# Kernel optimization log

Hardware: AMD Instinct MI355X
Metric: run time of the kernel (lower is better)

## Reference

```python
import jax, jax.numpy as jnp
import numpy as np

# Fixed quadtree structure for these inputs: base_size=192 => min=12, max=48.
# Level 1 (h=96 > max=48) always partitions; level 2 (h=48) never does because
# binarized uniform uncertainty has density ~0.99 > threshold 0.2.
# => 16 leaf windows of S=48 (N=2304 tokens each), identical to a 4x4 tiling.
B, D, H, W, S = 1, 64, 192, 192, 48
NEG = -1e10


def _to_windows(t, s):
    # [B,C,H,W] -> [B*(H//s)*(W//s), s*s, C]
    b, c, h, w = t.shape
    return t.reshape(b, c, h // s, s, w // s, s).transpose(0, 2, 4, 3, 5, 1).reshape(b * (h // s) * (w // s), s * s, c)


def _from_windows(t, b, c, h, w, s):
    # inverse of _to_windows
    return t.reshape(b, h // s, w // s, s, s, c).transpose(0, 5, 1, 3, 2, 4).reshape(b, c, h, w)


def setup_inputs() -> dict:
    key = jax.random.key(0)
    ks = jax.random.split(key, 16)
    d = D
    sc = 0.1  # ~1/sqrt(d) init scale
    n = lambda k, shape: jax.random.normal(k, shape, jnp.float32) * sc
    return {
        "x": jax.random.normal(ks[0], (B, d, H, W), jnp.float32),
        "reference_features": jax.random.normal(ks[1], (B, d, H, W), jnp.float32),
        "uncertainty_map": jax.random.uniform(ks[2], (B, 1, H, W), jnp.float32),
        "in_proj_w": n(ks[3], (3 * d, d)),
        "in_proj_b": n(ks[4], (3 * d,)),
        "out_proj_w": n(ks[5], (d, d)),
        "out_proj_b": n(ks[6], (d,)),
        "w1": n(ks[7], (d, d)),
        "b1": n(ks[8], (d,)),
        "w3": n(ks[9], (d, d, 3, 3)),
        "b3": n(ks[10], (d,)),
        "w4": n(ks[11], (1, d, 1, 1)),
        "b4": n(ks[12], (1,)),
    }


def reference(x, reference_features, uncertainty_map, in_proj_w, in_proj_b,
              out_proj_w, out_proj_b, w1, b1, w3, b3, w4, b4):
    b, c, h, w = x.shape
    u_bin = jnp.where(uncertainty_map > 0.01, 1.0, 0.0)
    qi = _to_windows(x, S)                      # [BW, N, C]
    kv = _to_windows(reference_features, S)     # [BW, N, C]
    u = _to_windows(u_bin, S)[..., 0]           # [BW, N]

    # torch nn.MultiheadAttention (1 head, batch_first) with additive float mask
    wq, wk, wv = jnp.split(in_proj_w, 3, axis=0)
    bq, bk, bv = jnp.split(in_proj_b, 3, axis=0)
    q = qi @ wq.T + bq
    k = kv @ wk.T + bk
    v = kv @ wv.T + bv
    logits = jnp.einsum('bnd,bmd->bnm', q, k) / (float(c) ** 0.5)
    # attn_mask = -1e10 where outer(u,u) < 1 (i.e. either token not uncertain)
    logits = logits + jnp.where(u[:, :, None] * u[:, None, :] < 1.0, NEG, 0.0)
    attn = jax.nn.softmax(logits, axis=-1)
    o = jnp.einsum('bnm,bmd->bnd', attn, v)
    o = o @ out_proj_w.T + out_proj_b           # MHA out_proj
    o = o @ w1.T + b1                           # conv_out1 (Linear)

    refined = _from_windows(qi + o, b, c, h, w, S)  # residual add per window

    # conv_out3: 3x3 conv + ReLU
    r3 = jax.lax.conv_general_dilated(refined, w3, (1, 1), 'SAME',
                                      dimension_numbers=('NCHW', 'OIHW', 'NCHW'))
    r3 = jax.nn.relu(r3 + b3[None, :, None, None])
    # conv_out4: 1x1 conv -> out_channel
    out = jnp.einsum('bchw,oc->bohw', r3, w4[:, :, 0, 0]) + b4[None, :, None, None]

    # partition map: borders of every visited quadtree window (96- and 48-level)
    # are written to 0.6 for batch 0 only; 96-level borders are a subset of 48-level.
    idx = jnp.arange(h)
    border = (idx % S == 0) | (idx % S == S - 1)
    pm0 = jnp.where(border[:, None] | border[None, :], 0.6, 1.0)
    partition_map = jnp.ones((b, 1, h, w), jnp.float32).at[0, 0].set(pm0)

    return (r3, out, partition_map)
```

## Files before the change

kernel.cpp:

```cpp
#include <hip/hip_runtime.h>
#include <hip/hip_bf16.h>

typedef unsigned char  u8_t;
typedef unsigned short u16_t;
typedef unsigned int   u32_t;
typedef __attribute__((ext_vector_type(8))) short bf16x8;
typedef __attribute__((ext_vector_type(4))) float f32x4;
typedef __attribute__((ext_vector_type(16))) float f32x16;

#define HW2  36864
#define NTOK 2304

__device__ __forceinline__ u32_t cvtpk(float a, float b) {
    union { __hip_bfloat162 h; u32_t u; } c;
    c.h = __float22bfloat162_rn(float2{a, b});
    return c.u;
}
__device__ __forceinline__ float bfhi(u32_t u) { union { u32_t u; float f; } c; c.u = u & 0xffff0000u; return c.f; }
__device__ __forceinline__ float bflo(u32_t u) { union { u32_t u; float f; } c; c.u = u << 16; return c.f; }

union U8x { u32_t u[4]; bf16x8 v; };

#define MF32(A, B, C) __builtin_amdgcn_mfma_f32_32x32x16_bf16(A, B, C, 0, 0, 0)

__global__ __launch_bounds__(256) void proj_kernel(
    const float* __restrict__ x, const float* __restrict__ ref, const float* __restrict__ unc,
    const float* __restrict__ ipw, const float* __restrict__ ipb,
    u16_t* __restrict__ Q, u16_t* __restrict__ K, u16_t* __restrict__ Vt, float* __restrict__ Uf)
{
    __shared__ u32_t Tt[64][33];
    const int side = blockIdx.x & 1;
    const int hb = blockIdx.x >> 1;
    const int bid = (hb & 7) * 72 + (hb >> 3);
    const int tokb = bid * 64;
    const int win = tokb / NTOK;
    const int n0 = tokb - win * NTOK;

    const int w = threadIdx.x >> 6;
    const int lane = threadIdx.x & 63;
    const int tile = w & 1;
    const int sel = w >> 1;
    const int q = lane & 31;
    const int hi = lane >> 5;

    const float* in = side ? ref : x;
    int n = n0 + tile * 32 + q;
    int p = ((win >> 2) * 48 + n / 48) * 192 + (win & 3) * 48 + n % 48;

    bf16x8 bfr[4];
    #pragma unroll
    for (int kc = 0; kc < 4; ++kc) {
        float v[8];
        #pragma unroll
        for (int i = 0; i < 8; ++i) v[i] = in[(size_t)(kc * 16 + hi * 8 + i) * HW2 + p];
        U8x pk;
        #pragma unroll
        for (int j = 0; j < 4; ++j) pk.u[j] = cvtpk(v[2 * j], v[2 * j + 1]);
        bfr[kc] = pk.v;
    }

    if (side == 0) {
        const float SCL = 0.18033688011112043f;
        const int oct = sel;
        f32x16 acc;
        #pragma unroll
        for (int r = 0; r < 16; ++r)
            acc[r] = ipb[oct * 32 + (r & 3) + 8 * (r >> 2) + 4 * hi] * SCL;
        #pragma unroll
        for (int kc = 0; kc < 4; ++kc) {
            const float* wr = ipw + (size_t)(oct * 32 + q) * 64 + kc * 16 + hi * 8;
            U8x a;
            #pragma unroll
            for (int j = 0; j < 4; ++j) a.u[j] = cvtpk(wr[2 * j] * SCL, wr[2 * j + 1] * SCL);
            acc = MF32(a.v, bfr[kc], acc);
        }
        #pragma unroll
        for (int rp = 0; rp < 8; ++rp) {
            int j = (rp & 1) + ((rp >> 1) << 2) + 2 * hi + (oct << 4);
            Tt[tile * 32 + q][j] = cvtpk(acc[2 * rp], acc[2 * rp + 1]);
        }
    } else if (sel == 0) {
        #pragma unroll
        for (int oct = 0; oct < 2; ++oct) {
            f32x16 acc;
            #pragma unroll
            for (int r = 0; r < 16; ++r)
                acc[r] = ipb[64 + oct * 32 + (r & 3) + 8 * (r >> 2) + 4 * hi];
            #pragma unroll
            for (int kc = 0; kc < 4; ++kc) {
                const float* wr = ipw + (size_t)(64 + oct * 32 + q) * 64 + kc * 16 + hi * 8;
                U8x a;
                #pragma unroll
                for (int j = 0; j < 4; ++j) a.u[j] = cvtpk(wr[2 * j], wr[2 * j + 1]);
                acc = MF32(a.v, bfr[kc], acc);
            }
            #pragma unroll
            for (int rp = 0; rp < 8; ++rp) {
                int j = (rp & 1) + ((rp >> 1) << 2) + 2 * hi + (oct << 4);
                Tt[tile * 32 + q][j] = cvtpk(acc[2 * rp], acc[2 * rp + 1]);
            }
        }
    } else {
        int sub = (q >> 2) & 7;
        int pq = (((sub ^ (sub >> 1)) & 1) ? (q ^ 12) : q);
        u16_t* vb = Vt + (size_t)win * 64 * NTOK + n0 + tile * 32 + pq;
        #pragma unroll
        for (int oct = 0; oct < 2; ++oct) {
            f32x16 acc;
            #pragma unroll
            for (int r = 0; r < 16; ++r)
                acc[r] = ipb[128 + oct * 32 + (r & 3) + 8 * (r >> 2) + 4 * hi];
            #pragma unroll
            for (int kc = 0; kc < 4; ++kc) {
                const float* wr = ipw + (size_t)(128 + oct * 32 + q) * 64 + kc * 16 + hi * 8;
                U8x a;
                #pragma unroll
                for (int j = 0; j < 4; ++j) a.u[j] = cvtpk(wr[2 * j], wr[2 * j + 1]);
                acc = MF32(a.v, bfr[kc], acc);
            }
            #pragma unroll
            for (int r = 0; r < 16; ++r) {
                int ch = oct * 32 + (r & 3) + 8 * (r >> 2) + 4 * hi;
                vb[(size_t)ch * NTOK] = (u16_t)(cvtpk(acc[r], 0.f) & 0xffffu);
            }
        }
        if (hi == 0) Uf[tokb + tile * 32 + q] = (unc[p] > 0.01f) ? 0.f : -100.f;
    }
    __syncthreads();

    {
        u16_t* dst = side ? K : Q;
        int tok = threadIdx.x >> 2, s8 = (threadIdx.x & 3) * 8;
        u32_t v0[4], v1[4];
        #pragma unroll
        for (int j = 0; j < 4; ++j) { v0[j] = Tt[tok][s8 + j]; v1[j] = Tt[tok][s8 + 4 + j]; }
        u32_t* d = (u32_t*)(dst + (size_t)(tokb + tok) * 64) + s8;
        *(uint4*)d       = uint4{v0[0], v0[1], v0[2], v0[3]};
        *(uint4*)(d + 4) = uint4{v1[0], v1[1], v1[2], v1[3]};
    }
}

__global__ __launch_bounds__(256) void prepmv_kernel(
    const float* __restrict__ wop, const float* __restrict__ bop,
    const float* __restrict__ w1, const float* __restrict__ b1,
    const float* __restrict__ w3, const u16_t* __restrict__ Vt,
    float* __restrict__ Wc, float* __restrict__ bc, u16_t* __restrict__ Wpk,
    float* __restrict__ meanV)
{
    __shared__ float red[16][17];
    int tid = threadIdx.x;
    if (blockIdx.x == 0) {
        for (int idx = tid; idx < 4096; idx += 256) {
            int f = idx >> 6, d = idx & 63;
            float a = 0.f;
            for (int e = 0; e < 64; ++e) a += w1[f * 64 + e] * wop[e * 64 + d];
            Wc[idx] = a;
        }
        if (tid < 64) {
            float a = b1[tid];
            for (int e = 0; e < 64; ++e) a += w1[tid * 64 + e] * bop[e];
            bc[tid] = a;
        }
    } else if (blockIdx.x < 37) {
        for (int idx = (blockIdx.x - 1) * 256 + tid; idx < 36864; idx += 9216) {
            int i = idx & 7;
            int lane = (idx >> 3) & 63;
            int t2 = idx >> 9;
            int ks = t2 % 18, mf = t2 / 18;
            int oc = mf * 16 + (lane & 15);
            int g = lane >> 4;
            int tap = ks >> 1, icc = ks & 1;
            int dy = tap / 3, dx = tap - (tap / 3) * 3;
            int ic = icc * 32 + g * 8 + i;
            Wpk[idx] = (u16_t)(cvtpk(w3[(size_t)(oc * 64 + ic) * 9 + dy * 3 + dx], 0.f) & 0xffffu);
        }
    } else {
        int m = blockIdx.x - 37;
        int win = m >> 2, cq = m & 3;
        int chl = tid >> 4, seg = tid & 15;
        const uint2* src = (const uint2*)(Vt + (size_t)win * 64 * NTOK + (size_t)(cq * 16 + chl) * NTOK + seg * 144);
        float s = 0.f;
        for (int i = 0; i < 36; ++i) {
            uint2 v = src[i];
            s += bflo(v.x) + bfhi(v.x) + bflo(v.y) + bfhi(v.y);
        }
        red[chl][seg] = s;
        __syncthreads();
        if (tid < 16) {
            float a = 0.f;
            #pragma unroll
            for (int k = 0; k < 16; ++k) a += red[tid][k];
            meanV[win * 64 + cq * 16 + tid] = a * (1.f / 2304.f);
        }
    }
}

__global__ __launch_bounds__(256, 2) void attn_kernel(
    const u16_t* __restrict__ Q, const u16_t* __restrict__ K, const u16_t* __restrict__ Vt,
    const float* __restrict__ Uf, const float* __restrict__ meanV, u16_t* __restrict__ Oatt)
{
    __shared__ float Ored[4][32][68];
    __shared__ float Lred2[2][4][32];

    const int bid = (blockIdx.x & 7) * 72 + (blockIdx.x >> 3);
    const int lane = threadIdx.x & 63;
    const int kq = threadIdx.x >> 6;
    const int q  = lane & 31;
    const int hi = lane >> 5;
    const int win = bid / 36;
    const int rg  = bid % 36;
    const int row0 = rg * 64;

    const u16_t* Qw = Q + (size_t)win * NTOK * 64;
    const u16_t* Kw = K + (size_t)win * NTOK * 64;
    const u16_t* Vw = Vt + (size_t)win * 64 * NTOK;
    const float* Uw = Uf + win * NTOK;

    bf16x8 qb0[4], qb1[4];
    #pragma unroll
    for (int s = 0; s < 4; ++s) {
        qb0[s] = *(const bf16x8*)(Qw + (size_t)(row0 + q) * 64 + s * 16 + hi * 8);
        qb1[s] = *(const bf16x8*)(Qw + (size_t)(row0 + 32 + q) * 64 + s * 16 + hi * 8);
    }

    const f32x16 Z16 = {0.f,0.f,0.f,0.f,0.f,0.f,0.f,0.f,0.f,0.f,0.f,0.f,0.f,0.f,0.f,0.f};
    f32x16 acc00 = Z16, acc01 = Z16, acc10 = Z16, acc11 = Z16;
    float lsum0 = 0.f, lsum1 = 0.f;

    const u16_t* kp = Kw + (size_t)(kq * 576 + q) * 64 + hi * 8;
    const u16_t* vp = Vw + (size_t)q * NTOK + kq * 576 + hi * 8;
    const float* up = Uw + kq * 576 + 4 * hi;

    bf16x8 kA0,kA1,kA2,kA3, vA0,vA1,vA2,vA3;
    bf16x8 kB0,kB1,kB2,kB3, vB0,vB1,vB2,vB3;
    float4 bA[4], bB[4];

#define LDSET(sfx, CT) { \
    const u16_t* _k = kp + (size_t)(CT) * 2048; \
    k##sfx##0 = *(const bf16x8*)(_k);      k##sfx##1 = *(const bf16x8*)(_k + 16); \
    k##sfx##2 = *(const bf16x8*)(_k + 32); k##sfx##3 = *(const bf16x8*)(_k + 48); \
    const u16_t* _v = vp + (CT) * 32; \
    v##sfx##0 = *(const bf16x8*)(_v);             v##sfx##1 = *(const bf16x8*)(_v + 16); \
    v##sfx##2 = *(const bf16x8*)(_v + 32 * NTOK); v##sfx##3 = *(const bf16x8*)(_v + 32 * NTOK + 16); \
    const float* _u = up + (CT) * 32; \
    b##sfx[0] = *(const float4*)(_u);      b##sfx[1] = *(const float4*)(_u + 8); \
    b##sfx[2] = *(const float4*)(_u + 16); b##sfx[3] = *(const float4*)(_u + 24); }

#define QS_TILE(sfx, QB, ACC0, ACC1, LSUM) { \
    f32x16 s; \
    s[0]  = b##sfx[0].x; s[1]  = b##sfx[0].y; s[2]  = b##sfx[0].z; s[3]  = b##sfx[0].w; \
    s[4]  = b##sfx[1].x; s[5]  = b##sfx[1].y; s[6]  = b##sfx[1].z; s[7]  = b##sfx[1].w; \
    s[8]  = b##sfx[2].x; s[9]  = b##sfx[2].y; s[10] = b##sfx[2].z; s[11] = b##sfx[2].w; \
    s[12] = b##sfx[3].x; s[13] = b##sfx[3].y; s[14] = b##sfx[3].z; s[15] = b##sfx[3].w; \
    s = MF32(k##sfx##0, QB[0], s); s = MF32(k##sfx##1, QB[1], s); \
    s = MF32(k##sfx##2, QB[2], s); s = MF32(k##sfx##3, QB[3], s); \
    float pv[16]; float lls = 0.f; \
    _Pragma("unroll") for (int r = 0; r < 16; ++r) { pv[r] = __builtin_exp2f(s[r]); lls += pv[r]; } \
    LSUM += lls; \
    U8x f0, f1; \
    _Pragma("unroll") for (int j = 0; j < 4; ++j) { \
        f0.u[j] = cvtpk(pv[2 * j], pv[2 * j + 1]); \
        f1.u[j] = cvtpk(pv[8 + 2 * j], pv[8 + 2 * j + 1]); } \
    ACC0 = MF32(v##sfx##0, f0.v, ACC0); ACC0 = MF32(v##sfx##1, f1.v, ACC0); \
    ACC1 = MF32(v##sfx##2, f0.v, ACC1); ACC1 = MF32(v##sfx##3, f1.v, ACC1); }

#define BODY(sfx) { QS_TILE(sfx, qb0, acc00, acc01, lsum0) QS_TILE(sfx, qb1, acc10, acc11, lsum1) }

    LDSET(A, 0)
    #pragma unroll 1
    for (int tt = 0; tt < 9; ++tt) {
        LDSET(B, 2 * tt + 1)
        BODY(A)
        if (tt < 8) LDSET(A, 2 * tt + 2)
        BODY(B)
    }
#undef BODY
#undef QS_TILE
#undef LDSET

    float l0 = lsum0 + __shfl_xor(lsum0, 32);
    float l1 = lsum1 + __shfl_xor(lsum1, 32);
    if (hi == 0) { Lred2[0][kq][q] = l0; Lred2[1][kq][q] = l1; }

    const int qr = threadIdx.x >> 3;
    const int ch0 = (threadIdx.x & 7) * 8;

    #pragma unroll
    for (int qs = 0; qs < 2; ++qs) {
        f32x16 a0 = qs ? acc10 : acc00;
        f32x16 a1 = qs ? acc11 : acc01;
        #pragma unroll
        for (int rr = 0; rr < 4; ++rr) {
            float4 v0 = { a0[4*rr], a0[4*rr+1], a0[4*rr+2], a0[4*rr+3] };
            float4 v1 = { a1[4*rr], a1[4*rr+1], a1[4*rr+2], a1[4*rr+3] };
            *(float4*)&Ored[kq][q][8 * rr + 4 * hi]      = v0;
            *(float4*)&Ored[kq][q][32 + 8 * rr + 4 * hi] = v1;
        }
        __syncthreads();
        float o[8] = {0.f,0.f,0.f,0.f,0.f,0.f,0.f,0.f};
        #pragma unroll
        for (int w = 0; w < 4; ++w) {
            float4 a = *(float4*)&Ored[w][qr][ch0];
            float4 b = *(float4*)&Ored[w][qr][ch0 + 4];
            o[0] += a.x; o[1] += a.y; o[2] += a.z; o[3] += a.w;
            o[4] += b.x; o[5] += b.y; o[6] += b.z; o[7] += b.w;
        }
        float l = Lred2[qs][0][qr] + Lred2[qs][1][qr] + Lred2[qs][2][qr] + Lred2[qs][3][qr];
        float linv = (l > 0.f) ? 1.f / l : 0.f;
        int row = row0 + 32 * qs + qr;
        uint4 wv;
        if (Uw[row] == 0.f) {
            wv = uint4{ cvtpk(o[0]*linv, o[1]*linv), cvtpk(o[2]*linv, o[3]*linv),
                        cvtpk(o[4]*linv, o[5]*linv), cvtpk(o[6]*linv, o[7]*linv) };
        } else {
            const float* mv = meanV + win * 64 + ch0;
            wv = uint4{ cvtpk(mv[0], mv[1]), cvtpk(mv[2], mv[3]),
                        cvtpk(mv[4], mv[5]), cvtpk(mv[6], mv[7]) };
        }
        *(uint4*)(Oatt + (size_t)(win * NTOK + row) * 64 + ch0) = wv;
        __syncthreads();
    }
}

__global__ __launch_bounds__(256) void refined_kernel(
    const float* __restrict__ x, const u16_t* __restrict__ Oatt,
    const float* __restrict__ Wc, const float* __restrict__ bc,
    u16_t* __restrict__ refd)
{
    __shared__ u32_t Tt[64][33];
    const int bid = (blockIdx.x & 7) * 72 + (blockIdx.x >> 3);
    const int tokb = bid * 64;
    const int win = tokb / NTOK;
    const int n0 = tokb - win * NTOK;

    const int w = threadIdx.x >> 6;
    const int lane = threadIdx.x & 63;
    const int tile = w & 1;
    const int oct = w >> 1;
    const int q = lane & 31;
    const int hi = lane >> 5;

    int n = n0 + tile * 32 + q;
    int p = ((win >> 2) * 48 + n / 48) * 192 + (win & 3) * 48 + n % 48;

    const u16_t* ob = Oatt + (size_t)(tokb + tile * 32 + q) * 64 + hi * 8;
    bf16x8 bfr[4];
    #pragma unroll
    for (int kc = 0; kc < 4; ++kc) bfr[kc] = *(const bf16x8*)(ob + kc * 16);

    f32x16 acc;
    #pragma unroll
    for (int r = 0; r < 16; ++r)
        acc[r] = bc[oct * 32 + (r & 3) + 8 * (r >> 2) + 4 * hi];
    #pragma unroll
    for (int kc = 0; kc < 4; ++kc) {
        const float* wr = Wc + (size_t)(oct * 32 + q) * 64 + kc * 16 + hi * 8;
        U8x a;
        #pragma unroll
        for (int j = 0; j < 4; ++j) a.u[j] = cvtpk(wr[2 * j], wr[2 * j + 1]);
        acc = MF32(a.v, bfr[kc], acc);
    }
    #pragma unroll
    for (int rp = 0; rp < 8; ++rp) {
        int ch = oct * 32 + (2 * rp & 3) + 8 * (rp >> 1) + 4 * hi;
        float xa = x[(size_t)ch * HW2 + p] + acc[2 * rp];
        float xb = x[(size_t)(ch + 1) * HW2 + p] + acc[2 * rp + 1];
        int j = (rp & 1) + ((rp >> 1) << 2) + 2 * hi + (oct << 4);
        Tt[tile * 32 + q][j] = cvtpk(xa, xb);
    }
    __syncthreads();

    {
        int tok = threadIdx.x >> 2, s8 = (threadIdx.x & 3) * 8;
        int nn = n0 + tok;
        int pp = ((win >> 2) * 48 + nn / 48) * 192 + (win & 3) * 48 + nn % 48;
        u32_t v0[4], v1[4];
        #pragma unroll
        for (int j = 0; j < 4; ++j) { v0[j] = Tt[tok][s8 + j]; v1[j] = Tt[tok][s8 + 4 + j]; }
        u32_t* d = (u32_t*)(refd + (size_t)pp * 64) + s8;
        *(uint4*)d       = uint4{v0[0], v0[1], v0[2], v0[3]};
        *(uint4*)(d + 4) = uint4{v1[0], v1[1], v1[2], v1[3]};
    }
}

__global__ __launch_bounds__(256) void conv_kernel(
    const u16_t* __restrict__ refined, const u16_t* __restrict__ Wpk,
    const float* __restrict__ b3, const float* __restrict__ w4, const float* __restrict__ b4,
    float* __restrict__ out0, float* __restrict__ out1, float* __restrict__ pm)
{
    __shared__ u16_t tile[3 * 50 * 64];
    __shared__ float ps[48];
    int bid = (blockIdx.x & 7) * 96 + (blockIdx.x >> 3);
    const int y  = bid >> 2;
    const int x0 = (bid & 3) * 48;
    const int tid = threadIdx.x;
    if (tid < 48) ps[tid] = 0.f;

    for (int idx = tid; idx < 1200; idx += 256) {
        int tg = idx & 7;
        int pix = idx >> 3;
        int r = pix / 50, cc = pix - r * 50;
        int yy = y - 1 + r, xg = x0 - 1 + cc;
        bf16x8 val = {0,0,0,0,0,0,0,0};
        if ((unsigned)yy < 192u && (unsigned)xg < 192u)
            val = *(const bf16x8*)(refined + ((size_t)(yy * 192 + xg)) * 64 + tg * 8);
        int slot = (tg + cc) & 7;
        *(bf16x8*)((char*)tile + (size_t)pix * 128 + slot * 16) = val;
    }
    __syncthreads();

    const int lane = tid & 63, mf = tid >> 6;
    const int ln = lane & 15, g = lane >> 4;

    bf16x8 wf[18];
    #pragma unroll
    for (int ks = 0; ks < 18; ++ks)
        wf[ks] = *(const bf16x8*)(Wpk + (size_t)((mf * 18 + ks) * 64 + lane) * 8);

    float b3v[4], w4v[4];
    #pragma unroll
    for (int r = 0; r < 4; ++r) { int oc = mf * 16 + 4 * g + r; b3v[r] = b3[oc]; w4v[r] = w4[oc]; }

    for (int nf = 0; nf < 3; ++nf) {
        int xl = nf * 16 + ln;
        f32x4 acc0 = {0.f,0.f,0.f,0.f}, acc1 = acc0;
        #pragma unroll
        for (int ks = 0; ks < 18; ++ks) {
            int tap = ks >> 1, icc = ks & 1;
            int dy = tap / 3, dx = tap - (tap / 3) * 3;
            int cc = xl + dx;
            int slot = (icc * 4 + g + cc) & 7;
            bf16x8 bfr = *(const bf16x8*)((const char*)tile + (size_t)(dy * 50 + cc) * 128 + slot * 16);
            if (ks & 1) acc1 = __builtin_amdgcn_mfma_f32_16x16x32_bf16(wf[ks], bfr, acc1, 0, 0, 0);
            else        acc0 = __builtin_amdgcn_mfma_f32_16x16x32_bf16(wf[ks], bfr, acc0, 0, 0, 0);
        }
        int xg = x0 + xl;
        float s4 = 0.f;
        #pragma unroll
        for (int r = 0; r < 4; ++r) {
            int oc = mf * 16 + 4 * g + r;
            float v = fmaxf(acc0[r] + acc1[r] + b3v[r], 0.f);
            out0[(size_t)oc * HW2 + y * 192 + xg] = v;
            s4 += v * w4v[r];
        }
        atomicAdd(&ps[xl], s4);
    }
    __syncthreads();
    if (tid < 48) {
        int xg = x0 + tid;
        out1[y * 192 + xg] = ps[tid] + b4[0];
        int ym = y % 48, xm = xg % 48;
        pm[y * 192 + xg] = ((ym == 0) | (ym == 47) | (xm == 0) | (xm == 47)) ? 0.6f : 1.0f;
    }
}

extern "C" void kernel_launch(void* const* d_in, const int* in_sizes, int n_in,
                              void* d_out, int out_size, void* d_ws, size_t ws_size,
                              hipStream_t stream)
{
    const float* x   = (const float*)d_in[0];
    const float* ref = (const float*)d_in[1];
    const float* unc = (const float*)d_in[2];
    const float* ipw = (const float*)d_in[3];
    const float* ipb = (const float*)d_in[4];
    const float* opw = (const float*)d_in[5];
    const float* opb = (const float*)d_in[6];
    const float* w1  = (const float*)d_in[7];
    const float* b1  = (const float*)d_in[8];
    const float* w3  = (const float*)d_in[9];
    const float* b3  = (const float*)d_in[10];
    const float* w4  = (const float*)d_in[11];
    const float* b4  = (const float*)d_in[12];

    char* ws = (char*)d_ws;
    u16_t* Qb    = (u16_t*)(ws);
    u16_t* Kb    = (u16_t*)(ws + 4718592);
    u16_t* Vtb   = (u16_t*)(ws + 9437184);
    float* Ufp   = (float*)(ws + 14155776);
    float* meanV = (float*)(ws + 14303232);
    float* Wc    = (float*)(ws + 14307328);
    float* bc    = (float*)(ws + 14323712);
    u16_t* Wpk   = (u16_t*)(ws + 14323968);
    u16_t* Oatt  = (u16_t*)(ws + 14397696);
    u16_t* refd  = (u16_t*)(ws + 19116288);

    float* out0 = (float*)d_out;
    float* out1 = out0 + 2359296;
    float* pmap = out0 + 2396160;

    proj_kernel   <<<1152, 256, 0, stream>>>(x, ref, unc, ipw, ipb, Qb, Kb, Vtb, Ufp);
    prepmv_kernel <<<101,  256, 0, stream>>>(opw, opb, w1, b1, w3, Vtb, Wc, bc, Wpk, meanV);
    attn_kernel   <<<576,  256, 0, stream>>>(Qb, Kb, Vtb, Ufp, meanV, Oatt);
    refined_kernel<<<576,  256, 0, stream>>>(x, Oatt, Wc, bc, refd);
    conv_kernel   <<<768,  256, 0, stream>>>(refd, Wpk, b3, w4, b4, out0, out1, pmap);
}
```

Measured before the change: 210.5 us.

## Split attention key range across two blocks and merge partials in refined kernel

The attention kernel now splits each window's 2304 keys into two halves handled by separate blocks, doubling the grid to 1152 blocks. Each block writes unnormalized bf16 partial outputs and row sums. The refined kernel adds the two partials, normalizes them, and applies the mean-V substitution for certain rows. The aim is more parallelism and occupancy in the dominant attention stage, at the cost of extra partial-result traffic and bf16 rounding of the unnormalized partials. The bias init also becomes a single vector union copy.

```diff
diff --git a/kernel.cpp b/kernel.cpp
--- a/kernel.cpp
+++ b/kernel.cpp
@@ -20,6 +20,7 @@
 __device__ __forceinline__ float bflo(u32_t u) { union { u32_t u; float f; } c; c.u = u << 16; return c.f; }
 
 union U8x { u32_t u[4]; bf16x8 v; };
+union F16x { float4 f4[4]; f32x16 v; };
 
 #define MF32(A, B, C) __builtin_amdgcn_mfma_f32_32x32x16_bf16(A, B, C, 0, 0, 0)
 
@@ -197,18 +198,20 @@
 
 __global__ __launch_bounds__(256, 2) void attn_kernel(
     const u16_t* __restrict__ Q, const u16_t* __restrict__ K, const u16_t* __restrict__ Vt,
-    const float* __restrict__ Uf, const float* __restrict__ meanV, u16_t* __restrict__ Oatt)
+    const float* __restrict__ Uf, u16_t* __restrict__ Opart, float* __restrict__ Lpart)
 {
     __shared__ float Ored[4][32][68];
     __shared__ float Lred2[2][4][32];
 
-    const int bid = (blockIdx.x & 7) * 72 + (blockIdx.x >> 3);
+    const int bid = (blockIdx.x & 7) * 144 + (blockIdx.x >> 3);
     const int lane = threadIdx.x & 63;
     const int kq = threadIdx.x >> 6;
     const int q  = lane & 31;
     const int hi = lane >> 5;
-    const int win = bid / 36;
-    const int rg  = bid % 36;
+    const int win = bid / 72;
+    const int rem = bid % 72;
+    const int rg   = rem >> 1;
+    const int half = rem & 1;
     const int row0 = rg * 64;
 
     const u16_t* Qw = Q + (size_t)win * NTOK * 64;
@@ -227,13 +230,14 @@
     f32x16 acc00 = Z16, acc01 = Z16, acc10 = Z16, acc11 = Z16;
     float lsum0 = 0.f, lsum1 = 0.f;
 
-    const u16_t* kp = Kw + (size_t)(kq * 576 + q) * 64 + hi * 8;
-    const u16_t* vp = Vw + (size_t)q * NTOK + kq * 576 + hi * 8;
-    const float* up = Uw + kq * 576 + 4 * hi;
+    const int cbase = half * 1152 + kq * 288;
+    const u16_t* kp = Kw + (size_t)(cbase + q) * 64 + hi * 8;
+    const u16_t* vp = Vw + (size_t)q * NTOK + cbase + hi * 8;
+    const float* up = Uw + cbase + 4 * hi;
 
     bf16x8 kA0,kA1,kA2,kA3, vA0,vA1,vA2,vA3;
     bf16x8 kB0,kB1,kB2,kB3, vB0,vB1,vB2,vB3;
-    float4 bA[4], bB[4];
+    F16x bA, bB;
 
 #define LDSET(sfx, CT) { \
     const u16_t* _k = kp + (size_t)(CT) * 2048; \
@@ -243,15 +247,11 @@
     v##sfx##0 = *(const bf16x8*)(_v);             v##sfx##1 = *(const bf16x8*)(_v + 16); \
     v##sfx##2 = *(const bf16x8*)(_v + 32 * NTOK); v##sfx##3 = *(const bf16x8*)(_v + 32 * NTOK + 16); \
     const float* _u = up + (CT) * 32; \
-    b##sfx[0] = *(const float4*)(_u);      b##sfx[1] = *(const float4*)(_u + 8); \
-    b##sfx[2] = *(const float4*)(_u + 16); b##sfx[3] = *(const float4*)(_u + 24); }
+    b##sfx.f4[0] = *(const float4*)(_u);      b##sfx.f4[1] = *(const float4*)(_u + 8); \
+    b##sfx.f4[2] = *(const float4*)(_u + 16); b##sfx.f4[3] = *(const float4*)(_u + 24); }
 
 #define QS_TILE(sfx, QB, ACC0, ACC1, LSUM) { \
-    f32x16 s; \
-    s[0]  = b##sfx[0].x; s[1]  = b##sfx[0].y; s[2]  = b##sfx[0].z; s[3]  = b##sfx[0].w; \
-    s[4]  = b##sfx[1].x; s[5]  = b##sfx[1].y; s[6]  = b##sfx[1].z; s[7]  = b##sfx[1].w; \
-    s[8]  = b##sfx[2].x; s[9]  = b##sfx[2].y; s[10] = b##sfx[2].z; s[11] = b##sfx[2].w; \
-    s[12] = b##sfx[3].x; s[13] = b##sfx[3].y; s[14] = b##sfx[3].z; s[15] = b##sfx[3].w; \
+    f32x16 s = b##sfx.v; \
     s = MF32(k##sfx##0, QB[0], s); s = MF32(k##sfx##1, QB[1], s); \
     s = MF32(k##sfx##2, QB[2], s); s = MF32(k##sfx##3, QB[3], s); \
     float pv[16]; float lls = 0.f; \
@@ -268,12 +268,13 @@
 
     LDSET(A, 0)
     #pragma unroll 1
-    for (int tt = 0; tt < 9; ++tt) {
+    for (int tt = 0; tt < 4; ++tt) {
         LDSET(B, 2 * tt + 1)
         BODY(A)
-        if (tt < 8) LDSET(A, 2 * tt + 2)
+        LDSET(A, 2 * tt + 2)
         BODY(B)
     }
+    BODY(A)
 #undef BODY
 #undef QS_TILE
 #undef LDSET
@@ -284,6 +285,8 @@
 
     const int qr = threadIdx.x >> 3;
     const int ch0 = (threadIdx.x & 7) * 8;
+    u16_t* Op = Opart + (size_t)half * 2359296;
+    float* Lp = Lpart + half * 36864;
 
     #pragma unroll
     for (int qs = 0; qs < 2; ++qs) {
@@ -305,25 +308,21 @@
             o[0] += a.x; o[1] += a.y; o[2] += a.z; o[3] += a.w;
             o[4] += b.x; o[5] += b.y; o[6] += b.z; o[7] += b.w;
         }
-        float l = Lred2[qs][0][qr] + Lred2[qs][1][qr] + Lred2[qs][2][qr] + Lred2[qs][3][qr];
-        float linv = (l > 0.f) ? 1.f / l : 0.f;
         int row = row0 + 32 * qs + qr;
-        uint4 wv;
-        if (Uw[row] == 0.f) {
-            wv = uint4{ cvtpk(o[0]*linv, o[1]*linv), cvtpk(o[2]*linv, o[3]*linv),
-                        cvtpk(o[4]*linv, o[5]*linv), cvtpk(o[6]*linv, o[7]*linv) };
-        } else {
-            const float* mv = meanV + win * 64 + ch0;
-            wv = uint4{ cvtpk(mv[0], mv[1]), cvtpk(mv[2], mv[3]),
-                        cvtpk(mv[4], mv[5]), cvtpk(mv[6], mv[7]) };
-        }
-        *(uint4*)(Oatt + (size_t)(win * NTOK + row) * 64 + ch0) = wv;
+        uint4 wv = uint4{ cvtpk(o[0], o[1]), cvtpk(o[2], o[3]),
+                          cvtpk(o[4], o[5]), cvtpk(o[6], o[7]) };
+        *(uint4*)(Op + (size_t)(win * NTOK + row) * 64 + ch0) = wv;
+        if ((threadIdx.x & 7) == 0) {
+            float l = Lred2[qs][0][qr] + Lred2[qs][1][qr] + Lred2[qs][2][qr] + Lred2[qs][3][qr];
+            Lp[win * NTOK + row] = l;
+        }
         __syncthreads();
     }
 }
 
 __global__ __launch_bounds__(256) void refined_kernel(
-    const float* __restrict__ x, const u16_t* __restrict__ Oatt,
+    const float* __restrict__ x, const u16_t* __restrict__ Opart, const float* __restrict__ Lpart,
+    const float* __restrict__ Uf, const float* __restrict__ meanV,
     const float* __restrict__ Wc, const float* __restrict__ bc,
     u16_t* __restrict__ refd)
 {
@@ -342,11 +341,35 @@
 
     int n = n0 + tile * 32 + q;
     int p = ((win >> 2) * 48 + n / 48) * 192 + (win & 3) * 48 + n % 48;
-
-    const u16_t* ob = Oatt + (size_t)(tokb + tile * 32 + q) * 64 + hi * 8;
+    int t = tokb + tile * 32 + q;
+
+    float l = Lpart[t] + Lpart[36864 + t];
+    float linv = (l > 0.f) ? 1.f / l : 0.f;
+    bool certain = (Uf[t] != 0.f);
+    const u16_t* p0 = Opart + (size_t)t * 64 + hi * 8;
+    const u16_t* p1 = p0 + 2359296;
+    const float* mv = meanV + win * 64 + hi * 8;
+
     bf16x8 bfr[4];
     #pragma unroll
-    for (int kc = 0; kc < 4; ++kc) bfr[kc] = *(const bf16x8*)(ob + kc * 16);
+    for (int kc = 0; kc < 4; ++kc) {
+        U8x ua, ub, uo;
+        ua.v = *(const bf16x8*)(p0 + kc * 16);
+        ub.v = *(const bf16x8*)(p1 + kc * 16);
+        if (!certain) {
+            #pragma unroll
+            for (int j = 0; j < 4; ++j) {
+                float s0 = (bflo(ua.u[j]) + bflo(ub.u[j])) * linv;
+                float s1 = (bfhi(ua.u[j]) + bfhi(ub.u[j])) * linv;
+                uo.u[j] = cvtpk(s0, s1);
+            }
+        } else {
+            const float* m = mv + kc * 16;
+            #pragma unroll
+            for (int j = 0; j < 4; ++j) uo.u[j] = cvtpk(m[2 * j], m[2 * j + 1]);
+        }
+        bfr[kc] = uo.v;
+    }
 
     f32x16 acc;
     #pragma unroll
@@ -481,8 +504,9 @@
     float* Wc    = (float*)(ws + 14307328);
     float* bc    = (float*)(ws + 14323712);
     u16_t* Wpk   = (u16_t*)(ws + 14323968);
-    u16_t* Oatt  = (u16_t*)(ws + 14397696);
-    u16_t* refd  = (u16_t*)(ws + 19116288);
+    u16_t* Opart = (u16_t*)(ws + 14397696);
+    float* Lpart = (float*)(ws + 23834880);
+    u16_t* refd  = (u16_t*)(ws + 24129792);
 
     float* out0 = (float*)d_out;
     float* out1 = out0 + 2359296;
@@ -490,7 +514,7 @@
 
     proj_kernel   <<<1152, 256, 0, stream>>>(x, ref, unc, ipw, ipb, Qb, Kb, Vtb, Ufp);
     prepmv_kernel <<<101,  256, 0, stream>>>(opw, opb, w1, b1, w3, Vtb, Wc, bc, Wpk, meanV);
-    attn_kernel   <<<576,  256, 0, stream>>>(Qb, Kb, Vtb, Ufp, meanV, Oatt);
-    refined_kernel<<<576,  256, 0, stream>>>(x, Oatt, Wc, bc, refd);
+    attn_kernel   <<<1152, 256, 0, stream>>>(Qb, Kb, Vtb, Ufp, Opart, Lpart);
+    refined_kernel<<<576,  256, 0, stream>>>(x, Opart, Lpart, Ufp, meanV, Wc, bc, refd);
     conv_kernel   <<<768,  256, 0, stream>>>(refd, Wpk, b3, w4, b4, out0, out1, pmap);
 }
```

After: 207.2 us. No clear change (-1.6%).
